# Kernel optimization log

Hardware: AMD Instinct MI355X
Metric: run time of the kernel (lower is better)

## Reference

```python
import jax, jax.numpy as jnp
import numpy as np
from jax import lax

IN_CH = 256
NF = 128
B, H, W = 8, 256, 256


def _bn_relu(y, s, b):
    # inference-mode BatchNorm folded into per-channel affine, then ReLU
    return jax.nn.relu(y * s[None, :, None, None] + b[None, :, None, None])


def _upsample_bilinear_ac(x, scale):
    # bilinear upsample, align_corners=True (matches torch nn.Upsample)
    b, c, h, w = x.shape
    Ho, Wo = h * scale, w * scale
    ys = jnp.arange(Ho, dtype=x.dtype) * ((h - 1) / (Ho - 1))
    xs = jnp.arange(Wo, dtype=x.dtype) * ((w - 1) / (Wo - 1))
    y0 = jnp.floor(ys).astype(jnp.int32)
    x0 = jnp.floor(xs).astype(jnp.int32)
    y1 = jnp.minimum(y0 + 1, h - 1)
    x1 = jnp.minimum(x0 + 1, w - 1)
    wy = (ys - y0.astype(x.dtype))[None, None, :, None]
    wx = (xs - x0.astype(x.dtype))[None, None, None, :]
    # interpolate rows then columns
    top = x[:, :, y0, :] * (1 - wy) + x[:, :, y1, :] * wy      # [b,c,Ho,w]
    out = top[:, :, :, x0] * (1 - wx) + top[:, :, :, x1] * wx  # [b,c,Ho,Wo]
    return out


def setup_inputs() -> dict:
    key = jax.random.key(0)
    ks = jax.random.split(key, 6)
    inp = {
        "x": jax.random.normal(ks[0], (B, 64, H, W), dtype=jnp.float32),
        "w1": jax.random.normal(ks[1], (IN_CH, 64, 8, 8), dtype=jnp.float32) * 0.02,
        "bn1_s": jnp.ones((IN_CH,), jnp.float32),
        "bn1_b": jnp.zeros((IN_CH,), jnp.float32),
        "w_fai": jax.random.normal(ks[2], (NF, IN_CH), dtype=jnp.float32) * 0.05,
        "bnf_s": jnp.ones((NF,), jnp.float32),
        "bnf_b": jnp.zeros((NF,), jnp.float32),
        "w_sit": jax.random.normal(ks[3], (NF, IN_CH), dtype=jnp.float32) * 0.05,
        "bns_s": jnp.ones((NF,), jnp.float32),
        "bns_b": jnp.zeros((NF,), jnp.float32),
        "w_gama": jax.random.normal(ks[4], (NF, IN_CH), dtype=jnp.float32) * 0.05,
        "bng_s": jnp.ones((NF,), jnp.float32),
        "bng_b": jnp.zeros((NF,), jnp.float32),
    }
    return inp


def reference(x, w1, bn1_s, bn1_b, w_fai, bnf_s, bnf_b, w_sit, bns_s, bns_b,
              w_gama, bng_s, bng_b):
    # conv1: 8x8 stride-8 conv, BN, ReLU  -> [B, IN_CH, h, w]
    y = lax.conv_general_dilated(x, w1, window_strides=(8, 8), padding="VALID",
                                 dimension_numbers=("NCHW", "OIHW", "NCHW"))
    y = _bn_relu(y, bn1_s, bn1_b)
    b, c, h, w = y.shape
    n = h * w
    # 1x1 conv projections (einsum), BN, ReLU
    fai = _bn_relu(jnp.einsum("bchw,oc->bohw", y, w_fai), bnf_s, bnf_b)
    sit = _bn_relu(jnp.einsum("bchw,oc->bohw", y, w_sit), bns_s, bns_b)
    gama = _bn_relu(jnp.einsum("bchw,oc->bohw", y, w_gama), bng_s, bng_b)
    fai = fai.reshape(b, NF, n)
    sit = sit.reshape(b, NF, n)
    gama = gama.reshape(b, NF, n)
    # non-local attention: sigmoid(fai^T sit) @ gama^T
    sf = jax.nn.sigmoid(jnp.einsum("bcn,bcm->bnm", fai, sit))  # [b, n, n]
    out = jnp.einsum("bnm,bcm->bcn", sf, gama)                  # [b, NF, n]
    out = out.reshape(b, NF, h, w)
    return _upsample_bilinear_ac(out, 8)
```

## Files before the change

### kernel.cpp

```cpp
#include <hip/hip_runtime.h>

typedef __attribute__((ext_vector_type(8))) short short8_t;
typedef __attribute__((ext_vector_type(4))) float float4_t;

__device__ __forceinline__ unsigned short f2bf(float f) {
    unsigned int u = __float_as_uint(f);
    return (unsigned short)((u + 0x7FFFu + ((u >> 16) & 1u)) >> 16);
}
__device__ __forceinline__ unsigned int pkbf(float a, float b) {
    return (unsigned int)f2bf(a) | ((unsigned int)f2bf(b) << 16);
}

__global__ __launch_bounds__(256) void k_wprep(
    const float* __restrict__ w1, unsigned short* __restrict__ w1s)
{
    const int id = blockIdx.x * 256 + threadIdx.x;
    const float4* s = (const float4*)(w1 + id * 8);
    float4 a = s[0], b = s[1];
    int4 o;
    o.x = pkbf(a.x, a.y); o.y = pkbf(a.z, a.w);
    o.z = pkbf(b.x, b.y); o.w = pkbf(b.z, b.w);
    *(int4*)(w1s + id * 8) = o;
}

#define CONV_LOAD_A(dst, k0q) {                                               \
    const int ic = (k0q) >> 6, kh0 = ((k0q) >> 3) & 7;                        \
    const int xr = (oh0 + ohl) * 8 + kh0 + khl;                               \
    const float4* s4 = (const float4*)(x + (((bi * 64 + ic) * 256 + xr) * 256 + segA * 16)); \
    dst[0] = s4[0]; dst[1] = s4[1]; dst[2] = s4[2]; dst[3] = s4[3];           \
}
#define CONV_LOAD_B(dst, k0q) {                                               \
    _Pragma("unroll")                                                         \
    for (int l = 0; l < 4; ++l) {                                             \
        const int slot = l * 256 + tA;                                        \
        const int row = slot >> 2, p = slot & 3;                              \
        dst[l] = *(const int4*)(w1s + row * 4096 + (k0q) + p * 8);            \
    }                                                                         \
}
#define CONV_COMMIT_A(src) {                                                  \
    int4 p0, p1;                                                              \
    p0.x = pkbf(src[0].x, src[0].y); p0.y = pkbf(src[0].z, src[0].w);         \
    p0.z = pkbf(src[1].x, src[1].y); p0.w = pkbf(src[1].z, src[1].w);         \
    p1.x = pkbf(src[2].x, src[2].y); p1.y = pkbf(src[2].z, src[2].w);         \
    p1.z = pkbf(src[3].x, src[3].y); p1.w = pkbf(src[3].z, src[3].w);         \
    *(int4*)&At[rowA * 40 + koffA] = p0;                                      \
    *(int4*)&At[(rowA + 1) * 40 + koffA] = p1;                                \
}
#define CONV_COMMIT_B(src) {                                                  \
    _Pragma("unroll")                                                         \
    for (int l = 0; l < 4; ++l) {                                             \
        const int slot = l * 256 + tA;                                        \
        const int row = slot >> 2, p = slot & 3;                              \
        *(int4*)&Bt[row * 40 + p * 8] = src[l];                               \
    }                                                                         \
}
#define CONV_MFMA() {                                                         \
    short8_t aF[4], bF[4];                                                    \
    _Pragma("unroll")                                                         \
    for (int i = 0; i < 4; ++i) {                                             \
        const int R = wm * 64 + i * 16 + r16;                                 \
        aF[i] = *(const short8_t*)&At[R * 40 + (quad ^ ((r16 >> 1) & 3)) * 8];\
    }                                                                         \
    _Pragma("unroll")                                                         \
    for (int j = 0; j < 4; ++j)                                               \
        bF[j] = *(const short8_t*)&Bt[(wn * 64 + j * 16 + r16) * 40 + quad * 8]; \
    _Pragma("unroll")                                                         \
    for (int i = 0; i < 4; ++i)                                               \
        _Pragma("unroll")                                                     \
        for (int j = 0; j < 4; ++j)                                           \
            acc[i][j] = __builtin_amdgcn_mfma_f32_16x16x32_bf16(aF[i], bF[j], acc[i][j], 0, 0, 0); \
}

__global__ __launch_bounds__(512, 2) void k_conv1(
    const float* __restrict__ x, const unsigned short* __restrict__ w1s,
    float* __restrict__ part)
{
    __shared__ unsigned short At[128 * 40];
    __shared__ unsigned short Bt[256 * 40];
    const int tid = threadIdx.x;
    const int mt = blockIdx.x, kc = blockIdx.y;
    const int m0 = mt * 128;
    const int bi = mt >> 3;
    const int oh0 = (mt & 7) * 4;
    const int lane = tid & 63, wid = tid >> 6;
    const int wm = wid & 1, wn = wid >> 1;
    const int quad = lane >> 4, r16 = lane & 15;
    const bool isA = tid < 256;
    const int tA = tid & 255;
    const int rA = tA >> 4, segA = tA & 15;
    const int ohl = rA >> 2, khl = rA & 3;
    const int rowA = ohl * 32 + segA * 2;
    const int koffA = (khl ^ (segA & 3)) * 8;
    const int kbase = kc * 1024;
    float4_t acc[4][4] = {};
    float4 raA[4], raB[4];
    int4 rbA[4], rbB[4];

    if (isA) { CONV_LOAD_A(raA, kbase); CONV_LOAD_A(raB, kbase + 32); }
    else     { CONV_LOAD_B(rbA, kbase); CONV_LOAD_B(rbB, kbase + 32); }

    for (int it = 0; it < 32; it += 2) {
        if (isA) CONV_COMMIT_A(raA) else CONV_COMMIT_B(rbA);
        __syncthreads();
        if (it + 2 < 32) {
            const int k0 = kbase + (it + 2) * 32;
            if (isA) CONV_LOAD_A(raA, k0) else CONV_LOAD_B(rbA, k0);
        }
        CONV_MFMA();
        __syncthreads();
        if (isA) CONV_COMMIT_A(raB) else CONV_COMMIT_B(rbB);
        __syncthreads();
        if (it + 3 < 32) {
            const int k0 = kbase + (it + 3) * 32;
            if (isA) CONV_LOAD_A(raB, k0) else CONV_LOAD_B(rbB, k0);
        }
        CONV_MFMA();
        __syncthreads();
    }
    float* pp = part + ((size_t)kc << 21);
    #pragma unroll
    for (int i = 0; i < 4; ++i) {
        const int mg = m0 + wm * 64 + i * 16 + quad * 4;
        #pragma unroll
        for (int j = 0; j < 4; ++j) {
            const int ng = wn * 64 + j * 16 + r16;
            #pragma unroll
            for (int r = 0; r < 4; ++r)
                pp[(mg + r) * 256 + ng] = acc[i][j][r];
        }
    }
}

__global__ __launch_bounds__(256, 4) void k_reduce(
    const float* __restrict__ part, const float* __restrict__ s1,
    const float* __restrict__ b1, unsigned short* __restrict__ y)
{
    const int id = blockIdx.x * 256 + threadIdx.x;
    const int c4 = id & 63;
    const float4* p = (const float4*)part + id;
    float4 a = p[0], b = p[524288], c = p[1048576], d = p[1572864];
    float4 s = ((const float4*)s1)[c4], bb = ((const float4*)b1)[c4];
    float vx = fmaxf((a.x + b.x + c.x + d.x) * s.x + bb.x, 0.f);
    float vy = fmaxf((a.y + b.y + c.y + d.y) * s.y + bb.y, 0.f);
    float vz = fmaxf((a.z + b.z + c.z + d.z) * s.z + bb.z, 0.f);
    float vw = fmaxf((a.w + b.w + c.w + d.w) * s.w + bb.w, 0.f);
    int2 o; o.x = pkbf(vx, vy); o.y = pkbf(vz, vw);
    ((int2*)y)[id] = o;
}

__global__ __launch_bounds__(256, 2) void k_proj3(
    const unsigned short* __restrict__ y,
    const float* __restrict__ w_fai, const float* __restrict__ w_sit,
    const float* __restrict__ w_gama,
    const float* __restrict__ fs, const float* __restrict__ fb,
    const float* __restrict__ ss, const float* __restrict__ sb,
    const float* __restrict__ gs, const float* __restrict__ gb,
    unsigned short* __restrict__ P, unsigned short* __restrict__ G)
{
    __shared__ unsigned short At[64 * 40];
    __shared__ unsigned short Bt[64 * 40];
    const int tid = threadIdx.x;
    const int nt = blockIdx.x, mt = blockIdx.y;
    const int m0 = mt * 64;
    const float *W, *S, *Bb;
    if (nt < 2)      { W = w_fai;  S = fs; Bb = fb; }
    else if (nt < 4) { W = w_sit;  S = ss; Bb = sb; }
    else             { W = w_gama; S = gs; Bb = gb; }
    const int roff = (nt * 64) & 127;
    const int lane = tid & 63, wid = tid >> 6;
    const int wm = wid & 1, wn = wid >> 1;
    const int quad = lane >> 4, r16 = lane & 15;
    float4_t acc[2][2] = {};

    for (int k0 = 0; k0 < 256; k0 += 32) {
        {
            const int row = tid >> 2, pp = tid & 3;
            *(int4*)&At[row * 40 + pp * 8] =
                *(const int4*)(y + (m0 + row) * 256 + k0 + pp * 8);
        }
        #pragma unroll
        for (int l = 0; l < 2; ++l) {
            const int slot = l * 256 + tid;
            const int row = slot >> 3, pp = slot & 7;
            float4 v = *(const float4*)(W + (roff + row) * 256 + k0 + pp * 4);
            int2 wv; wv.x = pkbf(v.x, v.y); wv.y = pkbf(v.z, v.w);
            *(int2*)&Bt[row * 40 + pp * 4] = wv;
        }
        __syncthreads();
        short8_t aF[2], bF[2];
        #pragma unroll
        for (int i = 0; i < 2; ++i)
            aF[i] = *(const short8_t*)&At[(wm * 32 + i * 16 + r16) * 40 + quad * 8];
        #pragma unroll
        for (int j = 0; j < 2; ++j)
            bF[j] = *(const short8_t*)&Bt[(wn * 32 + j * 16 + r16) * 40 + quad * 8];
        #pragma unroll
        for (int i = 0; i < 2; ++i)
            #pragma unroll
            for (int j = 0; j < 2; ++j)
                acc[i][j] = __builtin_amdgcn_mfma_f32_16x16x32_bf16(aF[i], bF[j], acc[i][j], 0, 0, 0);
        __syncthreads();
    }
    #pragma unroll
    for (int i = 0; i < 2; ++i) {
        const int mg = m0 + wm * 32 + i * 16 + quad * 4;
        #pragma unroll
        for (int j = 0; j < 2; ++j) {
            const int nl = wn * 32 + j * 16 + r16;
            const float sc = S[roff + nl], bc = Bb[roff + nl];
            if (nt < 4) {
                const int col = nt * 64 + nl;
                #pragma unroll
                for (int r = 0; r < 4; ++r) {
                    float v = fmaxf(acc[i][j][r] * sc + bc, 0.f);
                    P[(mg + r) * 256 + col] = f2bf(v);
                }
            } else {
                const int c = roff + nl;
                #pragma unroll
                for (int r = 0; r < 4; ++r) {
                    float v = fmaxf(acc[i][j][r] * sc + bc, 0.f);
                    const int sp = mg + r;
                    G[((sp >> 10) * 128 + c) * 1024 + (sp & 1023)] = f2bf(v);
                }
            }
        }
    }
}

#define LSTR 152
__global__ __launch_bounds__(256, 2) void k_attn(
    const unsigned short* __restrict__ P, const unsigned short* __restrict__ G,
    float* __restrict__ Opart)
{
    __shared__ unsigned short At[64 * LSTR];
    __shared__ unsigned short Bt[128 * LSTR];
    __shared__ unsigned short Sl[64 * LSTR];
    const int tid = threadIdx.x;
    const int nt = blockIdx.x, zz = blockIdx.y;
    const int b = zz >> 2, kc = zz & 3;
    const int n0 = nt * 64;
    const int base = b * 1024;
    const int lane = tid & 63, wid = tid >> 6;
    const int wm = wid & 1, wn = wid >> 1;
    const int quad = lane >> 4, r16 = lane & 15;
    const int srow = tid >> 4, sp16 = tid & 15;
    float4_t acc2[2][4] = {};
    int4 rs[8], rg[8];

    #pragma unroll
    for (int l = 0; l < 4; ++l) {
        const int slot = l * 256 + tid;
        const int row = slot >> 4, p = slot & 15;
        *(int4*)&At[row * LSTR + p * 8] =
            *(const int4*)(P + (base + n0 + row) * 256 + p * 8);
    }
    {
        const int m1 = kc * 256;
        #pragma unroll
        for (int l = 0; l < 8; ++l)
            rs[l] = *(const int4*)(P + (base + m1 + (l * 16 + srow)) * 256 + 128 + sp16 * 8);
    }
    #pragma unroll
    for (int ms = 0; ms < 2; ++ms) {
        const int m1 = kc * 256 + ms * 128;
        #pragma unroll
        for (int l = 0; l < 8; ++l)
            *(int4*)&Bt[(l * 16 + srow) * LSTR + sp16 * 8] = rs[l];
        __syncthreads();
        #pragma unroll
        for (int l = 0; l < 8; ++l)
            rg[l] = *(const int4*)(G + (b * 128 + (l * 16 + srow)) * 1024 + m1 + sp16 * 8);
        float4_t acc1[2][4] = {};
        #pragma unroll
        for (int c = 0; c < 4; ++c) {
            short8_t aF[2], bF[4];
            #pragma unroll
            for (int i = 0; i < 2; ++i)
                aF[i] = *(const short8_t*)&At[(wm * 32 + i * 16 + r16) * LSTR + c * 32 + quad * 8];
            #pragma unroll
            for (int j = 0; j < 4; ++j)
                bF[j] = *(const short8_t*)&Bt[(wn * 64 + j * 16 + r16) * LSTR + c * 32 + quad * 8];
            #pragma unroll
            for (int i = 0; i < 2; ++i)
                #pragma unroll
                for (int j = 0; j < 4; ++j)
                    acc1[i][j] = __builtin_amdgcn_mfma_f32_16x16x32_bf16(aF[i], bF[j], acc1[i][j], 0, 0, 0);
        }
        __syncthreads();
        #pragma unroll
        for (int i = 0; i < 2; ++i) {
            const int nl = wm * 32 + i * 16 + quad * 4;
            #pragma unroll
            for (int j = 0; j < 4; ++j) {
                const int ml = wn * 64 + j * 16 + r16;
                #pragma unroll
                for (int r = 0; r < 4; ++r) {
                    const float xv = acc1[i][j][r];
                    const float e = __expf(-xv);
                    const float v = __builtin_amdgcn_rcpf(1.0f + e);
                    Sl[(nl + r) * LSTR + ml] = f2bf(v);
                }
            }
        }
        #pragma unroll
        for (int l = 0; l < 8; ++l)
            *(int4*)&Bt[(l * 16 + srow) * LSTR + sp16 * 8] = rg[l];
        if (ms == 0) {
            const int m1n = kc * 256 + 128;
            #pragma unroll
            for (int l = 0; l < 8; ++l)
                rs[l] = *(const int4*)(P + (base + m1n + (l * 16 + srow)) * 256 + 128 + sp16 * 8);
        }
        __syncthreads();
        #pragma unroll
        for (int c = 0; c < 4; ++c) {
            short8_t aF[2], bF[4];
            #pragma unroll
            for (int i = 0; i < 2; ++i)
                aF[i] = *(const short8_t*)&Sl[(wm * 32 + i * 16 + r16) * LSTR + c * 32 + quad * 8];
            #pragma unroll
            for (int j = 0; j < 4; ++j)
                bF[j] = *(const short8_t*)&Bt[(wn * 64 + j * 16 + r16) * LSTR + c * 32 + quad * 8];
            #pragma unroll
            for (int i = 0; i < 2; ++i)
                #pragma unroll
                for (int j = 0; j < 4; ++j)
                    acc2[i][j] = __builtin_amdgcn_mfma_f32_16x16x32_bf16(aF[i], bF[j], acc2[i][j], 0, 0, 0);
        }
        __syncthreads();
    }
    float* op = Opart + (size_t)kc * 1048576 + (size_t)b * 131072;
    #pragma unroll
    for (int i = 0; i < 2; ++i) {
        const int nl = n0 + wm * 32 + i * 16 + quad * 4;
        #pragma unroll
        for (int j = 0; j < 4; ++j) {
            const int ch = wn * 64 + j * 16 + r16;
            #pragma unroll
            for (int r = 0; r < 4; ++r)
                op[(nl + r) * 128 + ch] = acc2[i][j][r];
        }
    }
}

__global__ __launch_bounds__(256, 2) void k_up(
    const float* __restrict__ Opart, float* __restrict__ out)
{
    __shared__ float l0[32 * 136];
    __shared__ float l1[32 * 136];
    const int tid = threadIdx.x;
    const int yb = blockIdx.x, b = blockIdx.y;
    const float sc = 31.0f / 255.0f;
    const float fy = yb * sc;
    const int y0 = (int)fy;
    const float wy = fy - (float)y0;
    const int y1 = (y0 + 1 < 32) ? y0 + 1 : 31;
    const float4* r0 = (const float4*)(Opart + (size_t)b * 131072 + y0 * 4096);
    const float4* r1 = (const float4*)(Opart + (size_t)b * 131072 + y1 * 4096);
    #pragma unroll
    for (int j = 0; j < 4; ++j) {
        const int id = j * 256 + tid;
        const int xs = id >> 5, c4 = id & 31;
        float4 a0 = r0[id], a1 = r1[id];
        #pragma unroll
        for (int kc = 1; kc < 4; ++kc) {
            float4 t0 = r0[id + kc * 262144], t1 = r1[id + kc * 262144];
            a0.x += t0.x; a0.y += t0.y; a0.z += t0.z; a0.w += t0.w;
            a1.x += t1.x; a1.y += t1.y; a1.z += t1.z; a1.w += t1.w;
        }
        *(float4*)(l0 + xs * 136 + c4 * 4) = a0;
        *(float4*)(l1 + xs * 136 + c4 * 4) = a1;
    }
    __syncthreads();
    const float fx = tid * sc;
    const int x0 = (int)fx;
    const float wx = fx - (float)x0;
    const int x1 = (x0 + 1 < 32) ? x0 + 1 : 31;
    const float w00 = (1.f - wy) * (1.f - wx), w01 = (1.f - wy) * wx;
    const float w10 = wy * (1.f - wx), w11 = wy * wx;
    const float* a = l0 + x0 * 136;
    const float* bq = l0 + x1 * 136;
    const float* c = l1 + x0 * 136;
    const float* d = l1 + x1 * 136;
    float* op = out + (size_t)b * 8388608 + yb * 256 + tid;
    #pragma unroll 4
    for (int ch = 0; ch < 128; ++ch)
        op[ch * 65536] = w00 * a[ch] + w01 * bq[ch] + w10 * c[ch] + w11 * d[ch];
}

extern "C" void kernel_launch(void* const* d_in, const int* in_sizes, int n_in,
                              void* d_out, int out_size, void* d_ws, size_t ws_size,
                              hipStream_t stream) {
    (void)in_sizes; (void)n_in; (void)out_size; (void)ws_size;
    const float* x      = (const float*)d_in[0];
    const float* w1     = (const float*)d_in[1];
    const float* bn1_s  = (const float*)d_in[2];
    const float* bn1_b  = (const float*)d_in[3];
    const float* w_fai  = (const float*)d_in[4];
    const float* bnf_s  = (const float*)d_in[5];
    const float* bnf_b  = (const float*)d_in[6];
    const float* w_sit  = (const float*)d_in[7];
    const float* bns_s  = (const float*)d_in[8];
    const float* bns_b  = (const float*)d_in[9];
    const float* w_gama = (const float*)d_in[10];
    const float* bng_s  = (const float*)d_in[11];
    const float* bng_b  = (const float*)d_in[12];
    float* out = (float*)d_out;

    char* ws = (char*)d_ws;
    float*          pc    = (float*)ws;
    float*          Opart = (float*)(ws + 16u * 1024 * 1024);
    unsigned short* y     = (unsigned short*)(ws + 32u * 1024 * 1024);
    unsigned short* P     = (unsigned short*)(ws + 36u * 1024 * 1024);
    unsigned short* G     = (unsigned short*)(ws + 40u * 1024 * 1024);
    unsigned short* w1s   = (unsigned short*)(ws + 44u * 1024 * 1024);

    k_wprep <<<dim3(512),      256, 0, stream>>>(w1, w1s);
    k_conv1 <<<dim3(64, 4),    512, 0, stream>>>(x, w1s, pc);
    k_reduce<<<dim3(2048),     256, 0, stream>>>(pc, bn1_s, bn1_b, y);
    k_proj3 <<<dim3(6, 128),   256, 0, stream>>>(y, w_fai, w_sit, w_gama,
                                                 bnf_s, bnf_b, bns_s, bns_b,
                                                 bng_s, bng_b, P, G);
    k_attn  <<<dim3(16, 32),   256, 0, stream>>>(P, G, Opart);
    k_up    <<<dim3(256, 8),   256, 0, stream>>>(Opart, out);
}
```

Measured before the change: 509.6 us.

## Double-buffer conv1 LDS tiles with single barrier per k-step; drop attn register prefetch

The conv1 GEMM now keeps two LDS buffers for A and B. Each k-step computes on one buffer while the next tile is written into the other, so only one barrier per step is needed instead of two. A custom barrier waits only on LDS counters. Occupancy drops from 2 to 1 blocks per CU, since the LDS footprint doubles and the launch bound changes. In k_attn, the register-staged prefetch of the P and G tiles is replaced with direct global-to-LDS copies at use time, which lowers register pressure but exposes global load latency.

```diff
diff --git a/kernel.cpp b/kernel.cpp
--- a/kernel.cpp
+++ b/kernel.cpp
@@ -10,6 +10,8 @@
 __device__ __forceinline__ unsigned int pkbf(float a, float b) {
     return (unsigned int)f2bf(a) | ((unsigned int)f2bf(b) << 16);
 }
+
+#define BARRIER_LGKM() asm volatile("s_waitcnt lgkmcnt(0)\ns_barrier" ::: "memory")
 
 __global__ __launch_bounds__(256) void k_wprep(
     const float* __restrict__ w1, unsigned short* __restrict__ w1s)
@@ -37,33 +39,33 @@
         dst[l] = *(const int4*)(w1s + row * 4096 + (k0q) + p * 8);            \
     }                                                                         \
 }
-#define CONV_COMMIT_A(src) {                                                  \
+#define CONV_COMMIT_A(Abuf, src) {                                            \
     int4 p0, p1;                                                              \
     p0.x = pkbf(src[0].x, src[0].y); p0.y = pkbf(src[0].z, src[0].w);         \
     p0.z = pkbf(src[1].x, src[1].y); p0.w = pkbf(src[1].z, src[1].w);         \
     p1.x = pkbf(src[2].x, src[2].y); p1.y = pkbf(src[2].z, src[2].w);         \
     p1.z = pkbf(src[3].x, src[3].y); p1.w = pkbf(src[3].z, src[3].w);         \
-    *(int4*)&At[rowA * 40 + koffA] = p0;                                      \
-    *(int4*)&At[(rowA + 1) * 40 + koffA] = p1;                                \
-}
-#define CONV_COMMIT_B(src) {                                                  \
+    *(int4*)&(Abuf)[rowA * 40 + koffA] = p0;                                  \
+    *(int4*)&(Abuf)[(rowA + 1) * 40 + koffA] = p1;                            \
+}
+#define CONV_COMMIT_B(Bbuf, src) {                                            \
     _Pragma("unroll")                                                         \
     for (int l = 0; l < 4; ++l) {                                             \
         const int slot = l * 256 + tA;                                        \
         const int row = slot >> 2, p = slot & 3;                              \
-        *(int4*)&Bt[row * 40 + p * 8] = src[l];                               \
+        *(int4*)&(Bbuf)[row * 40 + p * 8] = src[l];                           \
     }                                                                         \
 }
-#define CONV_MFMA() {                                                         \
+#define CONV_MFMA(Abuf, Bbuf) {                                               \
     short8_t aF[4], bF[4];                                                    \
     _Pragma("unroll")                                                         \
     for (int i = 0; i < 4; ++i) {                                             \
         const int R = wm * 64 + i * 16 + r16;                                 \
-        aF[i] = *(const short8_t*)&At[R * 40 + (quad ^ ((r16 >> 1) & 3)) * 8];\
+        aF[i] = *(const short8_t*)&(Abuf)[R * 40 + (quad ^ ((r16 >> 1) & 3)) * 8]; \
     }                                                                         \
     _Pragma("unroll")                                                         \
     for (int j = 0; j < 4; ++j)                                               \
-        bF[j] = *(const short8_t*)&Bt[(wn * 64 + j * 16 + r16) * 40 + quad * 8]; \
+        bF[j] = *(const short8_t*)&(Bbuf)[(wn * 64 + j * 16 + r16) * 40 + quad * 8]; \
     _Pragma("unroll")                                                         \
     for (int i = 0; i < 4; ++i)                                               \
         _Pragma("unroll")                                                     \
@@ -71,12 +73,12 @@
             acc[i][j] = __builtin_amdgcn_mfma_f32_16x16x32_bf16(aF[i], bF[j], acc[i][j], 0, 0, 0); \
 }
 
-__global__ __launch_bounds__(512, 2) void k_conv1(
+__global__ __launch_bounds__(512, 1) void k_conv1(
     const float* __restrict__ x, const unsigned short* __restrict__ w1s,
     float* __restrict__ part)
 {
-    __shared__ unsigned short At[128 * 40];
-    __shared__ unsigned short Bt[256 * 40];
+    __shared__ unsigned short At[2][128 * 40];
+    __shared__ unsigned short Bt[2][256 * 40];
     const int tid = threadIdx.x;
     const int mt = blockIdx.x, kc = blockIdx.y;
     const int m0 = mt * 128;
@@ -93,29 +95,35 @@
     const int koffA = (khl ^ (segA & 3)) * 8;
     const int kbase = kc * 1024;
     float4_t acc[4][4] = {};
-    float4 raA[4], raB[4];
-    int4 rbA[4], rbB[4];
-
-    if (isA) { CONV_LOAD_A(raA, kbase); CONV_LOAD_A(raB, kbase + 32); }
-    else     { CONV_LOAD_B(rbA, kbase); CONV_LOAD_B(rbB, kbase + 32); }
-
-    for (int it = 0; it < 32; it += 2) {
-        if (isA) CONV_COMMIT_A(raA) else CONV_COMMIT_B(rbA);
-        __syncthreads();
+    float4 sA0[4], sA1[4];
+    int4 sB0[4], sB1[4];
+
+    if (isA) { CONV_LOAD_A(sA0, kbase); CONV_LOAD_A(sA1, kbase + 32); }
+    else     { CONV_LOAD_B(sB0, kbase); CONV_LOAD_B(sB1, kbase + 32); }
+    if (isA) CONV_COMMIT_A(At[0], sA0) else CONV_COMMIT_B(Bt[0], sB0);
+    BARRIER_LGKM();
+
+    for (int it = 0; it < 32; ++it) {
+        const int cur = it & 1;
+        CONV_MFMA(At[cur], Bt[cur]);
+        if (it + 1 < 32) {
+            if (isA) {
+                if ((it + 1) & 1) CONV_COMMIT_A(At[1], sA1)
+                else              CONV_COMMIT_A(At[0], sA0)
+            } else {
+                if ((it + 1) & 1) CONV_COMMIT_B(Bt[1], sB1)
+                else              CONV_COMMIT_B(Bt[0], sB0)
+            }
+        }
         if (it + 2 < 32) {
             const int k0 = kbase + (it + 2) * 32;
-            if (isA) CONV_LOAD_A(raA, k0) else CONV_LOAD_B(rbA, k0);
-        }
-        CONV_MFMA();
-        __syncthreads();
-        if (isA) CONV_COMMIT_A(raB) else CONV_COMMIT_B(rbB);
-        __syncthreads();
-        if (it + 3 < 32) {
-            const int k0 = kbase + (it + 3) * 32;
-            if (isA) CONV_LOAD_A(raB, k0) else CONV_LOAD_B(rbB, k0);
-        }
-        CONV_MFMA();
-        __syncthreads();
+            if (isA) {
+                if (cur) CONV_LOAD_A(sA1, k0) else CONV_LOAD_A(sA0, k0);
+            } else {
+                if (cur) CONV_LOAD_B(sB1, k0) else CONV_LOAD_B(sB0, k0);
+            }
+        }
+        BARRIER_LGKM();
     }
     float* pp = part + ((size_t)kc << 21);
     #pragma unroll
@@ -244,9 +252,7 @@
     const int lane = tid & 63, wid = tid >> 6;
     const int wm = wid & 1, wn = wid >> 1;
     const int quad = lane >> 4, r16 = lane & 15;
-    const int srow = tid >> 4, sp16 = tid & 15;
     float4_t acc2[2][4] = {};
-    int4 rs[8], rg[8];
 
     #pragma unroll
     for (int l = 0; l < 4; ++l) {
@@ -255,22 +261,16 @@
         *(int4*)&At[row * LSTR + p * 8] =
             *(const int4*)(P + (base + n0 + row) * 256 + p * 8);
     }
-    {
-        const int m1 = kc * 256;
-        #pragma unroll
-        for (int l = 0; l < 8; ++l)
-            rs[l] = *(const int4*)(P + (base + m1 + (l * 16 + srow)) * 256 + 128 + sp16 * 8);
-    }
-    #pragma unroll
     for (int ms = 0; ms < 2; ++ms) {
         const int m1 = kc * 256 + ms * 128;
         #pragma unroll
-        for (int l = 0; l < 8; ++l)
-            *(int4*)&Bt[(l * 16 + srow) * LSTR + sp16 * 8] = rs[l];
-        __syncthreads();
-        #pragma unroll
-        for (int l = 0; l < 8; ++l)
-            rg[l] = *(const int4*)(G + (b * 128 + (l * 16 + srow)) * 1024 + m1 + sp16 * 8);
+        for (int l = 0; l < 8; ++l) {
+            const int slot = l * 256 + tid;
+            const int row = slot >> 4, p = slot & 15;
+            *(int4*)&Bt[row * LSTR + p * 8] =
+                *(const int4*)(P + (base + m1 + row) * 256 + 128 + p * 8);
+        }
+        __syncthreads();
         float4_t acc1[2][4] = {};
         #pragma unroll
         for (int c = 0; c < 4; ++c) {
@@ -304,13 +304,11 @@
             }
         }
         #pragma unroll
-        for (int l = 0; l < 8; ++l)
-            *(int4*)&Bt[(l * 16 + srow) * LSTR + sp16 * 8] = rg[l];
-        if (ms == 0) {
-            const int m1n = kc * 256 + 128;
-            #pragma unroll
-            for (int l = 0; l < 8; ++l)
-                rs[l] = *(const int4*)(P + (base + m1n + (l * 16 + srow)) * 256 + 128 + sp16 * 8);
+        for (int l = 0; l < 8; ++l) {
+            const int slot = l * 256 + tid;
+            const int row = slot >> 4, p = slot & 15;
+            *(int4*)&Bt[row * LSTR + p * 8] =
+                *(const int4*)(G + (b * 128 + row) * 1024 + m1 + p * 8);
         }
         __syncthreads();
         #pragma unroll
```

New measurement: 481.4 us. 5.5% less time.
